# Kernel tuning notes

Measured on AMD Instinct MI355X. Metric: run time of the kernel, lower is better.

The kernel has to match this reference:

```python
import jax, jax.numpy as jnp
import numpy as np

NUM_LABELS = 150
FEAT_DIM = 768
N_BALLS = 1500
BATCH = 256
BETA = 0.1
N_TRI = FEAT_DIM * (FEAT_DIM - 1) // 2


def _cdist(a, b):
    # Euclidean distance matrix [Na, Nb] without materializing [Na, Nb, D]
    a2 = jnp.sum(a * a, axis=1)[:, None]
    b2 = jnp.sum(b * b, axis=1)[None, :]
    d2 = jnp.maximum(a2 + b2 - 2.0 * (a @ b.T), 0.0)
    return jnp.sqrt(d2)


def _build_rotate_matrix(L, U, Dd):
    # shape='ellipsoid', triangle=False: strict lower tri <- L, strict upper tri <- U, diag <- Dd
    K, D = Dd.shape
    rows, cols = np.tril_indices(D, -1)  # rows > cols, matches torch.tril_indices(offset=-1)
    di = np.arange(D)
    R = jnp.zeros((K, D, D), dtype=Dd.dtype)
    R = R.at[:, rows, cols].set(L)
    R = R.at[:, cols, rows].set(U)
    R = R.at[:, di, di].set(Dd)
    return R


def setup_inputs() -> dict:
    key = jax.random.key(0)
    ks = jax.random.split(key, 8)
    pooled_output = jax.random.normal(ks[0], (BATCH, FEAT_DIM), jnp.float32)
    ood = jax.random.normal(ks[1], (BATCH, FEAT_DIM), jnp.float32)
    centroids = jax.random.normal(ks[2], (N_BALLS, FEAT_DIM), jnp.float32)
    delta = jax.random.uniform(ks[3], (N_BALLS,), jnp.float32, minval=0.5, maxval=2.0)
    L = 0.01 * jax.random.normal(ks[4], (NUM_LABELS, N_TRI), jnp.float32)
    U = 0.01 * jax.random.normal(ks[5], (NUM_LABELS, N_TRI), jnp.float32)
    Dd = jnp.ones((NUM_LABELS, FEAT_DIM), jnp.float32)
    labels = jax.random.randint(ks[6], (BATCH,), 0, NUM_LABELS)
    ball_labels = jnp.arange(N_BALLS) % NUM_LABELS  # 10 balls per class, no empty classes
    return dict(pooled_output=pooled_output, ood=ood, centroids=centroids, delta=delta,
                L=L, U=U, Dd=Dd, labels=labels, ball_labels=ball_labels)


def reference(pooled_output, ood, centroids, delta, L, U, Dd, labels, ball_labels):
    R = _build_rotate_matrix(L, U, Dd)  # [K, D, D]

    # --- assign nearest same-class ball ---
    dist_all = _cdist(pooled_output, centroids)  # [B, N]
    same_class = ball_labels[None, :] == labels[:, None]
    dist_all = jnp.where(same_class, dist_all, jnp.inf)
    ball_ids = jnp.argmin(dist_all, axis=1)  # [B]
    d = delta[ball_ids]
    c = centroids[ball_ids]
    cls = ball_labels[ball_ids]

    # --- rotate and boundary loss ---
    x = pooled_output - c  # [B, D]
    rotate_x = jnp.einsum('bij,bj->bi', R[cls], x)  # gathered bmm
    euc = jnp.linalg.norm(rotate_x, axis=1)  # [B]
    in_mask = d > euc
    pos_loss = jnp.where(in_mask, jnp.exp(euc - d), euc - d)
    pos_num = jnp.sum((euc > d).astype(jnp.float32))
    neg_num = jnp.sum((euc < d).astype(jnp.float32))

    # --- OOD branch: per-class nearest ball among that class's balls (vectorized over classes) ---
    dist_ood = _cdist(ood, centroids)  # [M, N]
    class_mask = ball_labels[None, :] == jnp.arange(NUM_LABELS)[:, None]  # [K, N]
    masked = jnp.where(class_mask[:, None, :], dist_ood[None, :, :], jnp.inf)  # [K, M, N]
    nearest = jnp.argmin(masked, axis=2)  # [K, M]
    c_near = centroids[nearest]  # [K, M, D]
    d_near = delta[nearest]  # [K, M]
    x_ood = ood[None, :, :] - c_near  # [K, M, D]
    rot_ood = jnp.einsum('kij,kmj->kmi', R, x_ood)  # [K, M, D]
    euc_ood = jnp.linalg.norm(rot_ood, axis=2)  # [K, M]
    in_ood = d_near > euc_ood
    contrib = jnp.where(in_ood, d_near - euc_ood + BETA, BETA * jnp.exp(d_near - euc_ood))
    neg_loss = jnp.sum(contrib, axis=0)  # [M], summed over classes as in the python loop

    pos_mean = jnp.mean(pos_loss)
    neg_mean = jnp.mean(neg_loss)
    loss = pos_mean + neg_mean
    return (pos_mean, neg_mean, pos_num, neg_num, loss)
```

## Files before the change

### kernel.cpp

```cpp
#include <hip/hip_runtime.h>

typedef short short8 __attribute__((ext_vector_type(8)));
typedef float floatx16 __attribute__((ext_vector_type(16)));
typedef unsigned short u16;

#define BATCH 256
#define FEAT 768
#define NBALLS 1500
#define NCLS 150
#define NTRI 294528
#define SN 1504
#define NCOL 320
#define NSLICE 12
#define BETA_C 0.1f

__device__ __forceinline__ u16 f2bf(float f) {
    unsigned u = __float_as_uint(f);
    return (u16)((u + 0x7FFFu + ((u >> 16) & 1u)) >> 16);
}
__device__ __forceinline__ unsigned pack2bf(float lo, float hi) {
    unsigned ul = __float_as_uint(lo); ul = (ul + 0x7FFFu + ((ul >> 16) & 1u)) >> 16;
    unsigned uh = __float_as_uint(hi); uh = (uh + 0x7FFFu + ((uh >> 16) & 1u)) & 0xFFFF0000u;
    return uh | ul;
}
__device__ __forceinline__ unsigned bf16sub2(unsigned a, unsigned b) {
    float lo = __uint_as_float(a << 16) - __uint_as_float(b << 16);
    float hi = __uint_as_float(a & 0xFFFF0000u) - __uint_as_float(b & 0xFFFF0000u);
    unsigned ul = __float_as_uint(lo); ul = (ul + 0x7FFFu + ((ul >> 16) & 1u)) >> 16;
    unsigned uh = __float_as_uint(hi); uh = (uh + 0x7FFFu + ((uh >> 16) & 1u)) & 0xFFFF0000u;
    return uh | ul;
}

__global__ __launch_bounds__(256) void k_prep(
    const float* __restrict__ pooled, const float* __restrict__ ood,
    const float* __restrict__ cent, const int* __restrict__ ball_labels,
    u16* __restrict__ xsrc, u16* __restrict__ cent_bf, float* __restrict__ cnorm,
    int* __restrict__ cls_cnt, int* __restrict__ cls_list,
    float* __restrict__ euc2_main, int* __restrict__ bcount) {
    __shared__ int scnt;
    const int t = threadIdx.x, blk = blockIdx.x;
    const int tid = blk * 256 + t, stride = gridDim.x * 256;
    uint2* xp = (uint2*)xsrc;
    for (int i = tid; i < (BATCH * FEAT) / 4; i += stride) {
        const float4 v = ((const float4*)pooled)[i];
        xp[i] = make_uint2(pack2bf(v.x, v.y), pack2bf(v.z, v.w));
    }
    uint2* xo = (uint2*)(xsrc + BATCH * FEAT);
    for (int i = tid; i < (BATCH * FEAT) / 4; i += stride) {
        const float4 v = ((const float4*)ood)[i];
        xo[i] = make_uint2(pack2bf(v.x, v.y), pack2bf(v.z, v.w));
    }
    uint2* cd = (uint2*)cent_bf;
    for (int i = tid; i < (NBALLS * FEAT) / 4; i += stride) {
        const float4 v = ((const float4*)cent)[i];
        cd[i] = make_uint2(pack2bf(v.x, v.y), pack2bf(v.z, v.w));
    }
    for (int i = tid; i < BATCH; i += stride) euc2_main[i] = 0.f;
    for (int i = tid; i < NCLS; i += stride) bcount[i] = 0;

    if (blk >= 512 && blk < 512 + 375) {
        int cid = (blk - 512) * 4 + (t >> 6);
        int lane = t & 63;
        const float* row = cent + (size_t)cid * FEAT;
        float s = 0.f;
#pragma unroll
        for (int q = 0; q < FEAT / 64; ++q) { float v = row[lane + q * 64]; s += v * v; }
        for (int o = 32; o > 0; o >>= 1) s += __shfl_down(s, o);
        if (lane == 0) cnorm[cid] = s;
    }
    if (blk >= 887 && blk < 887 + NCLS) {
        int k = blk - 887;
        if (t == 0) scnt = 0;
        __syncthreads();
        for (int n = t; n < NBALLS; n += 256) {
            if (ball_labels[n] == k) {
                int p = atomicAdd(&scnt, 1);
                if (p < 32) cls_list[k * 32 + p] = n;
            }
        }
        __syncthreads();
        if (t == 0) cls_cnt[k] = scnt < 32 ? scnt : 32;
    }
}

__global__ __launch_bounds__(256) void k_gemm_s(
    const u16* __restrict__ xsrc, const u16* __restrict__ cent_bf,
    const float* __restrict__ cnorm, float* __restrict__ S) {
    __shared__ u16 Aq[64 * 40];
    __shared__ u16 Bc[128 * 40];
    const int t = threadIdx.x;
    const int r0 = blockIdx.x * 64;
    const int n0 = blockIdx.y * 128;
    const int w = t >> 6, lane = t & 63;
    const int ml = lane & 31, kh = lane >> 5;
    const int rt = w & 1, cg = w >> 1;

    floatx16 acc[2];
#pragma unroll
    for (int ct = 0; ct < 2; ++ct)
#pragma unroll
        for (int e = 0; e < 16; ++e) acc[ct][e] = 0.f;

    const int ar = t >> 2, aj = (t & 3) * 8;
    const u16* asrc = xsrc + (size_t)(r0 + ar) * FEAT;
    const int bcn = t >> 1, bj = (t & 1) * 16;
    const int ng = n0 + bcn;
    const u16* bsrc = cent_bf + (size_t)(ng < NBALLS ? ng : 0) * FEAT;
    const bool bvalid = (ng < NBALLS);

#pragma unroll 1
    for (int k0 = 0; k0 < FEAT; k0 += 32) {
        uint4 av = *(const uint4*)(asrc + k0 + aj);
        uint4 b0, b1;
        if (bvalid) {
            b0 = *(const uint4*)(bsrc + k0 + bj);
            b1 = *(const uint4*)(bsrc + k0 + bj + 8);
        } else { b0 = make_uint4(0,0,0,0); b1 = make_uint4(0,0,0,0); }
        *(uint4*)&Aq[ar * 40 + aj] = av;
        *(uint4*)&Bc[bcn * 40 + bj] = b0;
        *(uint4*)&Bc[bcn * 40 + bj + 8] = b1;
        __syncthreads();
#pragma unroll
        for (int ks = 0; ks < 2; ++ks) {
            short8 a = *(const short8*)&Aq[(rt * 32 + ml) * 40 + ks * 16 + kh * 8];
#pragma unroll
            for (int ct = 0; ct < 2; ++ct) {
                short8 b = *(const short8*)&Bc[((cg * 2 + ct) * 32 + ml) * 40 + ks * 16 + kh * 8];
                acc[ct] = __builtin_amdgcn_mfma_f32_32x32x16_bf16(a, b, acc[ct], 0, 0, 0);
            }
        }
        __syncthreads();
    }
#pragma unroll
    for (int ct = 0; ct < 2; ++ct) {
        int colg = n0 + (cg * 2 + ct) * 32 + ml;
        if (colg >= SN) continue;
        float cn = (colg < NBALLS) ? cnorm[colg] : 0.f;
#pragma unroll
        for (int reg = 0; reg < 16; ++reg) {
            int row = (reg & 3) + 8 * (reg >> 2) + 4 * kh;
            int rgl = r0 + rt * 32 + row;
            S[(size_t)rgl * SN + colg] = cn - 2.f * acc[ct][reg];
        }
    }
}

__global__ void k_argmin(const float* __restrict__ S, const int* __restrict__ labels,
                         const int* __restrict__ cls_cnt, const int* __restrict__ cls_list,
                         int* __restrict__ ball_ids, int* __restrict__ bcount,
                         int* __restrict__ blist, int* __restrict__ nearidx) {
    const int t = threadIdx.x;
    if (blockIdx.x == 0) {
        int k = labels[t];
        if (k < 0) k = 0; if (k >= NCLS) k = NCLS - 1;
        int cnt = cls_cnt[k];
        float best = 3.4e38f; int bestn = 0;
        for (int i = 0; i < cnt; ++i) {
            int n = cls_list[k * 32 + i];
            float v = S[(size_t)t * SN + n];
            if (v < best) { best = v; bestn = n; }
        }
        ball_ids[t] = bestn;
        int slot = atomicAdd(&bcount[k], 1);
        if (slot < 64) blist[k * 64 + slot] = t;
    } else {
        int k = blockIdx.x - 1;
        int cnt = cls_cnt[k];
        float best = 3.4e38f; int bestn = 0;
        for (int i = 0; i < cnt; ++i) {
            int n = cls_list[k * 32 + i];
            float v = S[(size_t)(BATCH + t) * SN + n];
            if (v < best) { best = v; bestn = n; }
        }
        nearidx[k * BATCH + t] = bestn;
    }
}

__global__ __launch_bounds__(256, 2) void k_gemm2(
    const float* __restrict__ Lp, const float* __restrict__ Up, const float* __restrict__ Ddp,
    const u16* __restrict__ xsrc, const u16* __restrict__ cent_bf,
    const int* __restrict__ nearidx, const int* __restrict__ bcount,
    const int* __restrict__ blist, const int* __restrict__ ball_ids,
    float* __restrict__ euc2_part) {
    __shared__ u16 At[64 * 40];
    __shared__ u16 Bt[NCOL * 40];
    __shared__ unsigned oidx_s[NCOL];
    __shared__ unsigned cidx_s[NCOL];
    __shared__ float sred[2 * NCOL];

    const int t = threadIdx.x;
    const int slice = blockIdx.x;
    const int i0 = slice * 64;
    const int k = blockIdx.y;
    const float* __restrict__ Lr = Lp + (size_t)k * NTRI;
    const float* __restrict__ Ur = Up + (size_t)k * NTRI;
    const float* __restrict__ Ddr = Ddp + (size_t)k * FEAT;

    int bc = bcount[k]; if (bc > 64) bc = 64;
    oidx_s[t] = 256u + (unsigned)t;
    cidx_s[t] = (unsigned)nearidx[k * BATCH + t];
    if (t < 64) {
        unsigned oi = 0u, ci = 0xFFFFFFFFu;
        if (t < bc) { int b = blist[k * 64 + t]; oi = (unsigned)b; ci = (unsigned)ball_ids[b]; }
        oidx_s[256 + t] = oi;
        cidx_s[256 + t] = ci;
    }
    __syncthreads();

    const int w = t >> 6, lane = t & 63;
    const int ml = lane & 31, kh = lane >> 5;
    const int rt = w & 1, cg = w >> 1;

    floatx16 acc[5];
#pragma unroll
    for (int cc = 0; cc < 5; ++cc)
#pragma unroll
        for (int e = 0; e < 16; ++e) acc[cc][e] = 0.f;

    float a[8];
    auto loadA = [&](int j0) {
        if (j0 + 32 <= i0) {
#pragma unroll
            for (int u = 0; u < 2; ++u) {
                const int i = i0 + u * 32 + (t >> 3);
                const float* p = Lr + ((unsigned)(i * (i - 1)) >> 1) + j0 + (t & 7) * 4;
#pragma unroll
                for (int e = 0; e < 4; ++e) a[u * 4 + e] = p[e];
            }
        } else if (j0 >= i0 + 64) {
#pragma unroll
            for (int u = 0; u < 2; ++u) {
                const int j = j0 + u * 16 + (t >> 4);
                const float* p = Ur + ((unsigned)(j * (j - 1)) >> 1) + i0 + (t & 15) * 4;
#pragma unroll
                for (int e = 0; e < 4; ++e) a[u * 4 + e] = p[e];
            }
        } else {
#pragma unroll
            for (int u = 0; u < 8; ++u) {
                const int idx = u * 256 + t;
                const int i = i0 + (idx >> 5), jg = j0 + (idx & 31);
                float v;
                if (i > jg)      v = Lr[((unsigned)(i * (i - 1)) >> 1) + jg];
                else if (i < jg) v = Ur[((unsigned)(jg * (jg - 1)) >> 1) + i];
                else             v = Ddr[i];
                a[u] = v;
            }
        }
    };
    auto storeA = [&](int j0) {
        if (j0 + 32 <= i0) {
#pragma unroll
            for (int u = 0; u < 2; ++u) {
                const int row = u * 32 + (t >> 3);
                unsigned lo = pack2bf(a[u * 4 + 0], a[u * 4 + 1]);
                unsigned hi = pack2bf(a[u * 4 + 2], a[u * 4 + 3]);
                *(uint2*)&At[row * 40 + (t & 7) * 4] = make_uint2(lo, hi);
            }
        } else if (j0 >= i0 + 64) {
#pragma unroll
            for (int u = 0; u < 2; ++u) {
                const int jj = u * 16 + (t >> 4);
                const int ic = (t & 15) * 4;
#pragma unroll
                for (int e = 0; e < 4; ++e) At[(ic + e) * 40 + jj] = f2bf(a[u * 4 + e]);
            }
        } else {
#pragma unroll
            for (int u = 0; u < 8; ++u) {
                const int idx = u * 256 + t;
                At[(idx >> 5) * 40 + (idx & 31)] = f2bf(a[u]);
            }
        }
    };
    auto stageB = [&](int j0) {
#pragma unroll
        for (int u = 0; u < 5; ++u) {
            const int g = u * 256 + t;
            const int col = g >> 2, ch = (g & 3) * 8;
            const unsigned ci = cidx_s[col];
            u16* dst = &Bt[col * 40 + ch];
            if (ci == 0xFFFFFFFFu) {
                *(uint4*)dst = make_uint4(0u, 0u, 0u, 0u);
            } else {
                const u16* o = xsrc + (size_t)oidx_s[col] * FEAT + j0 + ch;
                const u16* c = cent_bf + (size_t)ci * FEAT + j0 + ch;
                const uint4 ov = *(const uint4*)o;
                const uint4 cv = *(const uint4*)c;
                uint4 rv;
                rv.x = bf16sub2(ov.x, cv.x); rv.y = bf16sub2(ov.y, cv.y);
                rv.z = bf16sub2(ov.z, cv.z); rv.w = bf16sub2(ov.w, cv.w);
                *(uint4*)dst = rv;
            }
        }
    };

    loadA(0);
#pragma unroll 1
    for (int j0 = 0; j0 < FEAT; j0 += 32) {
        storeA(j0);
        stageB(j0);
        __syncthreads();
        if (j0 + 32 < FEAT) loadA(j0 + 32);
#pragma unroll
        for (int ks = 0; ks < 2; ++ks) {
            const short8 af = *(const short8*)&At[(rt * 32 + ml) * 40 + ks * 16 + kh * 8];
#pragma unroll
            for (int cc = 0; cc < 5; ++cc) {
                const short8 bv = *(const short8*)&Bt[((cg * 5 + cc) * 32 + ml) * 40 + ks * 16 + kh * 8];
                acc[cc] = __builtin_amdgcn_mfma_f32_32x32x16_bf16(af, bv, acc[cc], 0, 0, 0);
            }
        }
        __syncthreads();
    }

#pragma unroll
    for (int cc = 0; cc < 5; ++cc) {
        float s = 0.f;
#pragma unroll
        for (int e = 0; e < 16; ++e) { float v = acc[cc][e]; s += v * v; }
        s += __shfl_xor(s, 32);
        if (kh == 0) sred[rt * NCOL + cg * 160 + cc * 32 + ml] = s;
    }
    __syncthreads();
    float* outp = euc2_part + ((size_t)k * NSLICE + slice) * NCOL;
    outp[t] = sred[t] + sred[NCOL + t];
    if (t < 64) outp[256 + t] = sred[256 + t] + sred[NCOL + 256 + t];
}

__global__ void k_reduce(const float* __restrict__ euc2_part, const int* __restrict__ bcount,
                         const int* __restrict__ blist,
                         float* __restrict__ euc2_ood, float* __restrict__ euc2_main) {
    const int k = blockIdx.x, t = threadIdx.x;
    const float* p = euc2_part + (size_t)k * NSLICE * NCOL;
    float s = 0.f;
#pragma unroll
    for (int s12 = 0; s12 < NSLICE; ++s12) s += p[s12 * NCOL + t];
    euc2_ood[k * BATCH + t] = s;
    if (t < 64) {
        int bc = bcount[k]; if (bc > 64) bc = 64;
        if (t < bc) {
            float s2 = 0.f;
#pragma unroll
            for (int s12 = 0; s12 < NSLICE; ++s12) s2 += p[s12 * NCOL + 256 + t];
            euc2_main[blist[k * 64 + t]] = s2;
        }
    }
}

__global__ void k_final(const float* __restrict__ euc2_main, const float* __restrict__ euc2_ood,
                        const int* __restrict__ ball_ids, const int* __restrict__ nearidx,
                        const float* __restrict__ delta, float* __restrict__ out) {
    __shared__ float red[256];
    const int t = threadIdx.x;

    float euc = sqrtf(euc2_main[t]);
    float d = delta[ball_ids[t]];
    float pl = (d > euc) ? expf(euc - d) : (euc - d);
    float pn = (euc > d) ? 1.f : 0.f;
    float nn = (euc < d) ? 1.f : 0.f;

    float s = 0.f;
    for (int k = 0; k < NCLS; ++k) {
        int idx = k * BATCH + t;
        float e = sqrtf(euc2_ood[idx]);
        float dn = delta[nearidx[idx]];
        s += (dn > e) ? (dn - e + BETA_C) : (BETA_C * expf(dn - e));
    }

    auto reduce = [&](float v) -> float {
        red[t] = v; __syncthreads();
        for (int o = 128; o > 0; o >>= 1) {
            if (t < o) red[t] += red[t + o];
            __syncthreads();
        }
        float r = red[0]; __syncthreads();
        return r;
    };
    float pos_sum = reduce(pl);
    float pnum    = reduce(pn);
    float nnum    = reduce(nn);
    float neg_sum = reduce(s);
    if (t == 0) {
        float pos_mean = pos_sum / (float)BATCH;
        float neg_mean = neg_sum / (float)BATCH;
        out[0] = pos_mean;
        out[1] = neg_mean;
        out[2] = pnum;
        out[3] = nnum;
        out[4] = pos_mean + neg_mean;
    }
}

extern "C" void kernel_launch(void* const* d_in, const int* in_sizes, int n_in,
                              void* d_out, int out_size, void* d_ws, size_t ws_size,
                              hipStream_t stream) {
    const float* pooled      = (const float*)d_in[0];
    const float* ood         = (const float*)d_in[1];
    const float* cent        = (const float*)d_in[2];
    const float* delta       = (const float*)d_in[3];
    const float* L           = (const float*)d_in[4];
    const float* U           = (const float*)d_in[5];
    const float* Dd          = (const float*)d_in[6];
    const int*   labels      = (const int*)d_in[7];
    const int*   ball_labels = (const int*)d_in[8];
    float* out = (float*)d_out;

    char* base = (char*)d_ws;
    size_t off = 0;
    auto carve = [&](size_t bytes) -> void* {
        off = (off + 255) & ~(size_t)255;
        void* p = base + off;
        off += bytes;
        return p;
    };
    u16*   xsrc      = (u16*)carve((size_t)512 * FEAT * 2);
    u16*   cent_bf   = (u16*)carve((size_t)NBALLS * FEAT * 2);
    float* cnorm     = (float*)carve((size_t)SN * 4);
    float* S         = (float*)carve((size_t)512 * SN * 4);
    int*   cls_cnt   = (int*)carve((size_t)NCLS * 4);
    int*   cls_list  = (int*)carve((size_t)NCLS * 32 * 4);
    int*   ball_ids  = (int*)carve((size_t)BATCH * 4);
    int*   bcount    = (int*)carve((size_t)NCLS * 4);
    int*   blist     = (int*)carve((size_t)NCLS * 64 * 4);
    int*   nearidx   = (int*)carve((size_t)NCLS * BATCH * 4);
    float* euc2_part = (float*)carve((size_t)NCLS * NSLICE * NCOL * 4);
    float* euc2_ood  = (float*)carve((size_t)NCLS * BATCH * 4);
    float* euc2_main = (float*)carve((size_t)BATCH * 4);

    k_prep<<<1037, 256, 0, stream>>>(pooled, ood, cent, ball_labels, xsrc, cent_bf, cnorm,
                                     cls_cnt, cls_list, euc2_main, bcount);
    k_gemm_s<<<dim3(8, 12), 256, 0, stream>>>(xsrc, cent_bf, cnorm, S);
    k_argmin<<<151, 256, 0, stream>>>(S, labels, cls_cnt, cls_list, ball_ids, bcount, blist, nearidx);
    k_gemm2<<<dim3(NSLICE, NCLS), 256, 0, stream>>>(L, U, Dd, xsrc, cent_bf,
                                                    nearidx, bcount, blist, ball_ids, euc2_part);
    k_reduce<<<NCLS, 256, 0, stream>>>(euc2_part, bcount, blist, euc2_ood, euc2_main);
    k_final<<<1, 256, 0, stream>>>(euc2_main, euc2_ood, ball_ids, nearidx, delta, out);
}
```

Measured before the change: 610.9 us.

## Widen GEMM K-tile to 64 with XOR-swizzled LDS and double-buffered A loads

The rotation GEMM now steps through the feature dimension in 64-wide chunks instead of 32, which halves the number of loop iterations and barriers. A and B tiles in LDS use an XOR chunk swizzle in place of row padding to avoid bank conflicts. The A-tile global loads go into two register buffers, with the next tile prefetched before the current one is stored. Launch bounds now ask for 3 blocks per CU, and the reduction buffer reuses Bt to save LDS. The trade-off is higher register pressure from the 2x16-float prefetch buffer while targeting more occupancy, which may cause spills.

```diff
diff --git a/kernel.cpp b/kernel.cpp
--- a/kernel.cpp
+++ b/kernel.cpp
@@ -29,6 +29,9 @@
     unsigned ul = __float_as_uint(lo); ul = (ul + 0x7FFFu + ((ul >> 16) & 1u)) >> 16;
     unsigned uh = __float_as_uint(hi); uh = (uh + 0x7FFFu + ((uh >> 16) & 1u)) & 0xFFFF0000u;
     return uh | ul;
+}
+__device__ __forceinline__ unsigned trioff(int x) {
+    return ((unsigned)x * (unsigned)(x - 1)) >> 1;
 }
 
 __global__ __launch_bounds__(256) void k_prep(
@@ -176,17 +179,16 @@
     }
 }
 
-__global__ __launch_bounds__(256, 2) void k_gemm2(
+__global__ __launch_bounds__(256, 3) void k_gemm2(
     const float* __restrict__ Lp, const float* __restrict__ Up, const float* __restrict__ Ddp,
     const u16* __restrict__ xsrc, const u16* __restrict__ cent_bf,
     const int* __restrict__ nearidx, const int* __restrict__ bcount,
     const int* __restrict__ blist, const int* __restrict__ ball_ids,
     float* __restrict__ euc2_part) {
-    __shared__ u16 At[64 * 40];
-    __shared__ u16 Bt[NCOL * 40];
+    __shared__ u16 At[64 * 64];
+    __shared__ u16 Bt[NCOL * 64];
     __shared__ unsigned oidx_s[NCOL];
     __shared__ unsigned cidx_s[NCOL];
-    __shared__ float sred[2 * NCOL];
 
     const int t = threadIdx.x;
     const int slice = blockIdx.x;
@@ -195,6 +197,100 @@
     const float* __restrict__ Lr = Lp + (size_t)k * NTRI;
     const float* __restrict__ Ur = Up + (size_t)k * NTRI;
     const float* __restrict__ Ddr = Ddp + (size_t)k * FEAT;
+
+    const int w = t >> 6, lane = t & 63;
+    const int ml = lane & 31, kh = lane >> 5;
+    const int rt = w & 1, cg = w >> 1;
+
+    float aL[2][16];
+    auto loadA = [&](int j0, int buf) {
+        if (j0 + 64 <= i0) {
+#pragma unroll
+            for (int u = 0; u < 2; ++u) {
+                const int g = u * 256 + t;
+                const int row = g >> 3, chunk = g & 7;
+                const float* p = Lr + trioff(i0 + row) + j0 + chunk * 8;
+#pragma unroll
+                for (int e = 0; e < 8; ++e) aL[buf][u * 8 + e] = p[e];
+            }
+        } else if (j0 >= i0 + 64) {
+#pragma unroll
+            for (int v = 0; v < 2; ++v) {
+                const int jj = (t >> 3) + 32 * v;
+                const float* p = Ur + trioff(j0 + jj) + i0 + (t & 7);
+#pragma unroll
+                for (int e = 0; e < 8; ++e) aL[buf][v * 8 + e] = p[8 * e];
+            }
+        } else {
+#pragma unroll
+            for (int u = 0; u < 16; ++u) {
+                const int idx = u * 256 + t;
+                const int row = idx >> 6, col = idx & 63;
+                const int i = i0 + row, jg = j0 + col;
+                float v;
+                if (i > jg)      v = Lr[trioff(i) + jg];
+                else if (i < jg) v = Ur[trioff(jg) + i];
+                else             v = Ddr[i];
+                aL[buf][u] = v;
+            }
+        }
+    };
+    auto storeA = [&](int j0, int buf) {
+        if (j0 + 64 <= i0) {
+#pragma unroll
+            for (int u = 0; u < 2; ++u) {
+                const int g = u * 256 + t;
+                const int row = g >> 3, chunk = g & 7;
+                uint4 rv;
+                rv.x = pack2bf(aL[buf][u*8+0], aL[buf][u*8+1]);
+                rv.y = pack2bf(aL[buf][u*8+2], aL[buf][u*8+3]);
+                rv.z = pack2bf(aL[buf][u*8+4], aL[buf][u*8+5]);
+                rv.w = pack2bf(aL[buf][u*8+6], aL[buf][u*8+7]);
+                *(uint4*)&At[row * 64 + ((chunk ^ (row & 7)) * 8)] = rv;
+            }
+        } else if (j0 >= i0 + 64) {
+#pragma unroll
+            for (int v = 0; v < 2; ++v) {
+                const int jj = (t >> 3) + 32 * v;
+                const int chunk = jj >> 3, pos = jj & 7;
+#pragma unroll
+                for (int e = 0; e < 8; ++e) {
+                    const int row = (t & 7) + 8 * e;
+                    At[row * 64 + ((chunk ^ (row & 7)) * 8) + pos] = f2bf(aL[buf][v * 8 + e]);
+                }
+            }
+        } else {
+#pragma unroll
+            for (int u = 0; u < 16; ++u) {
+                const int idx = u * 256 + t;
+                const int row = idx >> 6, col = idx & 63;
+                At[row * 64 + (((col >> 3) ^ (row & 7)) * 8) + (col & 7)] = f2bf(aL[buf][u]);
+            }
+        }
+    };
+    auto stageB = [&](int j0) {
+#pragma unroll
+        for (int u = 0; u < 10; ++u) {
+            const int g = u * 256 + t;
+            const int col = g >> 3, chunk = g & 7;
+            const unsigned ci = cidx_s[col];
+            u16* dst = &Bt[col * 64 + ((chunk ^ (col & 7)) * 8)];
+            if (ci == 0xFFFFFFFFu) {
+                *(uint4*)dst = make_uint4(0u, 0u, 0u, 0u);
+            } else {
+                const u16* o = xsrc + (size_t)oidx_s[col] * FEAT + j0 + chunk * 8;
+                const u16* c = cent_bf + (size_t)ci * FEAT + j0 + chunk * 8;
+                const uint4 ov = *(const uint4*)o;
+                const uint4 cv = *(const uint4*)c;
+                uint4 rv;
+                rv.x = bf16sub2(ov.x, cv.x); rv.y = bf16sub2(ov.y, cv.y);
+                rv.z = bf16sub2(ov.z, cv.z); rv.w = bf16sub2(ov.w, cv.w);
+                *(uint4*)dst = rv;
+            }
+        }
+    };
+
+    loadA(0, 0);
 
     int bc = bcount[k]; if (bc > 64) bc = 64;
     oidx_s[t] = 256u + (unsigned)t;
@@ -207,113 +303,36 @@
     }
     __syncthreads();
 
-    const int w = t >> 6, lane = t & 63;
-    const int ml = lane & 31, kh = lane >> 5;
-    const int rt = w & 1, cg = w >> 1;
-
     floatx16 acc[5];
 #pragma unroll
     for (int cc = 0; cc < 5; ++cc)
 #pragma unroll
         for (int e = 0; e < 16; ++e) acc[cc][e] = 0.f;
 
-    float a[8];
-    auto loadA = [&](int j0) {
-        if (j0 + 32 <= i0) {
-#pragma unroll
-            for (int u = 0; u < 2; ++u) {
-                const int i = i0 + u * 32 + (t >> 3);
-                const float* p = Lr + ((unsigned)(i * (i - 1)) >> 1) + j0 + (t & 7) * 4;
-#pragma unroll
-                for (int e = 0; e < 4; ++e) a[u * 4 + e] = p[e];
-            }
-        } else if (j0 >= i0 + 64) {
-#pragma unroll
-            for (int u = 0; u < 2; ++u) {
-                const int j = j0 + u * 16 + (t >> 4);
-                const float* p = Ur + ((unsigned)(j * (j - 1)) >> 1) + i0 + (t & 15) * 4;
-#pragma unroll
-                for (int e = 0; e < 4; ++e) a[u * 4 + e] = p[e];
-            }
-        } else {
-#pragma unroll
-            for (int u = 0; u < 8; ++u) {
-                const int idx = u * 256 + t;
-                const int i = i0 + (idx >> 5), jg = j0 + (idx & 31);
-                float v;
-                if (i > jg)      v = Lr[((unsigned)(i * (i - 1)) >> 1) + jg];
-                else if (i < jg) v = Ur[((unsigned)(jg * (jg - 1)) >> 1) + i];
-                else             v = Ddr[i];
-                a[u] = v;
-            }
-        }
-    };
-    auto storeA = [&](int j0) {
-        if (j0 + 32 <= i0) {
-#pragma unroll
-            for (int u = 0; u < 2; ++u) {
-                const int row = u * 32 + (t >> 3);
-                unsigned lo = pack2bf(a[u * 4 + 0], a[u * 4 + 1]);
-                unsigned hi = pack2bf(a[u * 4 + 2], a[u * 4 + 3]);
-                *(uint2*)&At[row * 40 + (t & 7) * 4] = make_uint2(lo, hi);
-            }
-        } else if (j0 >= i0 + 64) {
-#pragma unroll
-            for (int u = 0; u < 2; ++u) {
-                const int jj = u * 16 + (t >> 4);
-                const int ic = (t & 15) * 4;
-#pragma unroll
-                for (int e = 0; e < 4; ++e) At[(ic + e) * 40 + jj] = f2bf(a[u * 4 + e]);
-            }
-        } else {
-#pragma unroll
-            for (int u = 0; u < 8; ++u) {
-                const int idx = u * 256 + t;
-                At[(idx >> 5) * 40 + (idx & 31)] = f2bf(a[u]);
-            }
-        }
-    };
-    auto stageB = [&](int j0) {
-#pragma unroll
-        for (int u = 0; u < 5; ++u) {
-            const int g = u * 256 + t;
-            const int col = g >> 2, ch = (g & 3) * 8;
-            const unsigned ci = cidx_s[col];
-            u16* dst = &Bt[col * 40 + ch];
-            if (ci == 0xFFFFFFFFu) {
-                *(uint4*)dst = make_uint4(0u, 0u, 0u, 0u);
-            } else {
-                const u16* o = xsrc + (size_t)oidx_s[col] * FEAT + j0 + ch;
-                const u16* c = cent_bf + (size_t)ci * FEAT + j0 + ch;
-                const uint4 ov = *(const uint4*)o;
-                const uint4 cv = *(const uint4*)c;
-                uint4 rv;
-                rv.x = bf16sub2(ov.x, cv.x); rv.y = bf16sub2(ov.y, cv.y);
-                rv.z = bf16sub2(ov.z, cv.z); rv.w = bf16sub2(ov.w, cv.w);
-                *(uint4*)dst = rv;
-            }
-        }
-    };
-
-    loadA(0);
 #pragma unroll 1
-    for (int j0 = 0; j0 < FEAT; j0 += 32) {
-        storeA(j0);
+    for (int it = 0; it < FEAT / 64; ++it) {
+        const int j0 = it * 64;
+        const int buf = it & 1;
+        if (it + 1 < FEAT / 64) loadA(j0 + 64, buf ^ 1);
+        storeA(j0, buf);
         stageB(j0);
         __syncthreads();
-        if (j0 + 32 < FEAT) loadA(j0 + 32);
-#pragma unroll
-        for (int ks = 0; ks < 2; ++ks) {
-            const short8 af = *(const short8*)&At[(rt * 32 + ml) * 40 + ks * 16 + kh * 8];
+#pragma unroll
+        for (int ks = 0; ks < 4; ++ks) {
+            const int ch = ks * 2 + kh;
+            const int arow = rt * 32 + ml;
+            const short8 af = *(const short8*)&At[arow * 64 + ((ch ^ (arow & 7)) * 8)];
 #pragma unroll
             for (int cc = 0; cc < 5; ++cc) {
-                const short8 bv = *(const short8*)&Bt[((cg * 5 + cc) * 32 + ml) * 40 + ks * 16 + kh * 8];
+                const int brow = (cg * 5 + cc) * 32 + ml;
+                const short8 bv = *(const short8*)&Bt[brow * 64 + ((ch ^ (brow & 7)) * 8)];
                 acc[cc] = __builtin_amdgcn_mfma_f32_32x32x16_bf16(af, bv, acc[cc], 0, 0, 0);
             }
         }
         __syncthreads();
     }
 
+    float* sred = (float*)Bt;
 #pragma unroll
     for (int cc = 0; cc < 5; ++cc) {
         float s = 0.f;
```

New measurement: 819.7 us. +34.2%, slower.
